# Kernel tuning notes

Hardware: AMD Instinct MI355X
Metric: run time of the kernel (lower is better)

Reference implementation:

```python
import jax, jax.numpy as jnp
import numpy as np

N_NODES = 100000
F_DIM = 128
D_LAT = 64
N_EDGES = 1000000
H_DIM = 128


def setup_inputs() -> dict:
    key = jax.random.key(0)
    ks = jax.random.split(key, 10)
    rng = np.random.default_rng(0)
    # positive edges (random graph) and non-edge negative pairs (dedup vs edge set,
    # mirroring the membership check in the torch elbo loop)
    edges = rng.integers(0, N_NODES, size=(2, N_EDGES))
    edge_hash = edges[0].astype(np.int64) * N_NODES + edges[1]
    cand = rng.integers(0, N_NODES, size=(2, 2 * N_EDGES))
    cand_hash = cand[0].astype(np.int64) * N_NODES + cand[1]
    keep = ~np.isin(cand_hash, edge_hash)
    neg = cand[:, keep][:, :N_EDGES]
    r = lambda k, s, sc=1.0: jax.random.normal(k, s, jnp.float32) * sc
    return {
        "x": r(ks[0], (N_NODES, F_DIM)),
        "eps": r(ks[1], (N_NODES, D_LAT)),
        "W_mu": r(ks[2], (F_DIM, D_LAT), 0.05),
        "b_mu": jnp.zeros((D_LAT,), jnp.float32),
        "W_lv": r(ks[3], (F_DIM, D_LAT), 0.05),
        "b_lv": jnp.zeros((D_LAT,), jnp.float32),
        "W1": r(ks[4], (D_LAT, H_DIM), 0.1),
        "b1": jnp.zeros((H_DIM,), jnp.float32),
        "W2": r(ks[5], (H_DIM, 1), 0.1),
        "b2": jnp.zeros((1,), jnp.float32),
        "edge_index": jnp.asarray(edges, jnp.int64) if jax.config.jax_enable_x64 else jnp.asarray(edges, jnp.int32),
        "neg_index": jnp.asarray(neg, jnp.int64) if jax.config.jax_enable_x64 else jnp.asarray(neg, jnp.int32),
    }


def reference(x, eps, W_mu, b_mu, W_lv, b_lv, W1, b1, W2, b2, edge_index, neg_index):
    # encoder: per-node diagonal Gaussian q(z|x)
    mu = x @ W_mu + b_mu            # [N, D]
    logvar = x @ W_lv + b_lv        # [N, D]
    z = mu + eps * jnp.exp(0.5 * logvar)  # q.rsample()

    def pair_logits(idx):
        zu = z[idx[0]]              # [E, D] gather
        zv = z[idx[1]]
        h = jax.nn.relu((zu * zv) @ W1 + b1)  # [E, H]
        return (h @ W2 + b2)[:, 0]  # [E]

    # Bernoulli(logits).log_prob(1) = log_sigmoid(l); log(1 - sigmoid(l)) = log_sigmoid(-l)
    true_lp = jax.nn.log_sigmoid(pair_logits(edge_index))
    false_lp = jax.nn.log_sigmoid(-pair_logits(neg_index))
    recon = jnp.mean(jnp.concatenate([true_lp, false_lp]))

    # KL(q || N(0, I)) per node, mean over nodes
    kl = jnp.mean(0.5 * jnp.sum(jnp.square(mu) + jnp.exp(logvar) - 1.0 - logvar, axis=-1))
    return -(recon - kl)
```

## Files before the change

kernel.cpp:

```cpp
#include <hip/hip_runtime.h>
#include <math.h>

#define F_DIM 128
#define D_LAT 64
#define H_DIM 128

typedef __attribute__((ext_vector_type(8))) short bf16x8;
typedef __attribute__((ext_vector_type(4))) float f32x4;
typedef __attribute__((ext_vector_type(2))) float f32x2;
typedef __attribute__((ext_vector_type(2))) unsigned long long u64x2;

__device__ __forceinline__ unsigned short f2bf(float f) {
    unsigned int u = __builtin_bit_cast(unsigned int, f);
    return (unsigned short)((u + 0x8000u) >> 16);
}

#define GLDS16(gaddr, laddr)                                                        \
    __builtin_amdgcn_global_load_lds(                                               \
        (const __attribute__((address_space(1))) void*)(gaddr),                     \
        (__attribute__((address_space(3))) void*)(laddr), 16, 0, 0)

__device__ __forceinline__ long prod_fp8(unsigned long long qu, unsigned long long qv) {
    const unsigned int ul = (unsigned int)qu, uh = (unsigned int)(qu >> 32);
    const unsigned int vl = (unsigned int)qv, vh = (unsigned int)(qv >> 32);
    const f32x2 u01 = __builtin_amdgcn_cvt_pk_f32_fp8(ul, false);
    const f32x2 u23 = __builtin_amdgcn_cvt_pk_f32_fp8(ul, true);
    const f32x2 u45 = __builtin_amdgcn_cvt_pk_f32_fp8(uh, false);
    const f32x2 u67 = __builtin_amdgcn_cvt_pk_f32_fp8(uh, true);
    const f32x2 v01 = __builtin_amdgcn_cvt_pk_f32_fp8(vl, false);
    const f32x2 v23 = __builtin_amdgcn_cvt_pk_f32_fp8(vl, true);
    const f32x2 v45 = __builtin_amdgcn_cvt_pk_f32_fp8(vh, false);
    const f32x2 v67 = __builtin_amdgcn_cvt_pk_f32_fp8(vh, true);
    const f32x2 p01 = u01 * v01, p23 = u23 * v23;
    const f32x2 p45 = u45 * v45, p67 = u67 * v67;
    unsigned int r0 = __builtin_amdgcn_cvt_pk_fp8_f32(p01[0], p01[1], 0u, false);
    r0 = __builtin_amdgcn_cvt_pk_fp8_f32(p23[0], p23[1], r0, true);
    unsigned int r1 = __builtin_amdgcn_cvt_pk_fp8_f32(p45[0], p45[1], 0u, false);
    r1 = __builtin_amdgcn_cvt_pk_fp8_f32(p67[0], p67[1], r1, true);
    return (long)(((unsigned long long)r1 << 32) | r0);
}

__global__ __launch_bounds__(256) void enc_mfma_kernel(
    const float* __restrict__ x, const float* __restrict__ eps,
    const float* __restrict__ Wmu, const float* __restrict__ bmu,
    const float* __restrict__ Wlv, const float* __restrict__ blv,
    unsigned char* __restrict__ zb, float* __restrict__ accum, int nNodes)
{
    const int lane = threadIdx.x & 63;
    const int li   = lane & 15;
    const int gi   = lane >> 4;

    bf16x8 wf[8][4];
#pragma unroll
    for (int t = 0; t < 4; ++t)
#pragma unroll
        for (int s = 0; s < 4; ++s)
#pragma unroll
            for (int j = 0; j < 8; ++j) {
                const int k = s * 32 + gi * 8 + j;
                wf[t][s][j]     = (short)f2bf(Wmu[k * D_LAT + 16 * t + li]);
                wf[t + 4][s][j] = (short)f2bf(Wlv[k * D_LAT + 16 * t + li]);
            }
    float bmu4[4], blv4[4];
#pragma unroll
    for (int t = 0; t < 4; ++t) {
        bmu4[t] = bmu[16 * t + li];
        blv4[t] = blv[16 * t + li];
    }

    const int wid = (blockIdx.x * blockDim.x + threadIdx.x) >> 6;
    const int nw  = (gridDim.x * blockDim.x) >> 6;
    const int NB  = nNodes >> 4;

    float klacc = 0.f;
    for (int nb = wid; nb < NB; nb += nw) {
        const int nbase = nb << 4;
        const float* __restrict__ xrow = x + (size_t)(nbase + li) * F_DIM;

        bf16x8 af[4];
#pragma unroll
        for (int s = 0; s < 4; ++s) {
            const f32x4 v0 = *(const f32x4*)(xrow + s * 32 + gi * 8);
            const f32x4 v1 = *(const f32x4*)(xrow + s * 32 + gi * 8 + 4);
#pragma unroll
            for (int j = 0; j < 4; ++j) {
                af[s][j]     = (short)f2bf(v0[j]);
                af[s][j + 4] = (short)f2bf(v1[j]);
            }
        }

        f32x4 acc[8];
#pragma unroll
        for (int t = 0; t < 4; ++t) {
            acc[t]     = (f32x4){bmu4[t], bmu4[t], bmu4[t], bmu4[t]};
            acc[t + 4] = (f32x4){blv4[t], blv4[t], blv4[t], blv4[t]};
        }
#pragma unroll
        for (int t = 0; t < 8; ++t)
#pragma unroll
            for (int s = 0; s < 4; ++s)
                acc[t] = __builtin_amdgcn_mfma_f32_16x16x32_bf16(af[s], wf[t][s], acc[t], 0, 0, 0);

#pragma unroll
        for (int r = 0; r < 4; ++r) {
            const int row = nbase + gi * 4 + r;
#pragma unroll
            for (int t = 0; t < 4; ++t) {
                const float mu  = acc[t][r];
                const float lv  = acc[t + 4][r];
                const float e05 = __expf(0.5f * lv);
                klacc += mu * mu + e05 * e05 - 1.0f - lv;
                const float zv = fmaf(eps[(size_t)row * D_LAT + 16 * t + li], e05, mu);
                zb[(size_t)row * D_LAT + 16 * t + li] =
                    (unsigned char)(__builtin_amdgcn_cvt_pk_fp8_f32(zv, 0.f, 0u, false) & 0xffu);
            }
        }
    }
    for (int off = 32; off; off >>= 1) klacc += __shfl_xor(klacc, off);
    if (lane == 0) atomicAdd(&accum[1], 0.5f * klacc);
}

__global__ __launch_bounds__(512) void edge_mfma_kernel(
    const unsigned char* __restrict__ zb,
    const int* __restrict__ eidx, const int* __restrict__ nidx,
    const float* __restrict__ W1, const float* __restrict__ b1,
    const float* __restrict__ W2, const float* __restrict__ b2,
    float* __restrict__ accum, int E)
{
    __shared__ unsigned char sh[8][2][4][1024];

    const int lane = threadIdx.x & 63;
    const int li   = lane & 15;
    const int gi   = lane >> 4;
    const int w    = threadIdx.x >> 6;

    long w1q[8][2];
#pragma unroll
    for (int t = 0; t < 8; ++t)
#pragma unroll
        for (int s = 0; s < 2; ++s) {
            float f[8];
#pragma unroll
            for (int j = 0; j < 8; ++j)
                f[j] = W1[(gi * 16 + s * 8 + j) * H_DIM + 16 * t + li];
            unsigned int r0 = __builtin_amdgcn_cvt_pk_fp8_f32(f[0], f[1], 0u, false);
            r0 = __builtin_amdgcn_cvt_pk_fp8_f32(f[2], f[3], r0, true);
            unsigned int r1 = __builtin_amdgcn_cvt_pk_fp8_f32(f[4], f[5], 0u, false);
            r1 = __builtin_amdgcn_cvt_pk_fp8_f32(f[6], f[7], r1, true);
            w1q[t][s] = (long)(((unsigned long long)r1 << 32) | r0);
        }
    float b1r[8], w2r[8];
#pragma unroll
    for (int t = 0; t < 8; ++t) {
        b1r[t] = b1[16 * t + li];
        w2r[t] = W2[16 * t + li];
    }
    const float b2v = b2[0];

    const int wid = (blockIdx.x * blockDim.x + threadIdx.x) >> 6;
    const int nw  = (gridDim.x * blockDim.x) >> 6;
    const int NBpos = E >> 4;
    const int NBH   = NBpos;

    float lp = 0.f;

    auto load_idx = [&](int hb, int& u0, int& v0, int& u1, int& v1) {
        const int h   = (hb < NBH) ? hb : (NBH - 1);
        const int pb0 = 2 * h, pb1 = 2 * h + 1;
        const int* __restrict__ i0 = (pb0 < NBpos) ? eidx : nidx;
        const int* __restrict__ i1 = (pb1 < NBpos) ? eidx : nidx;
        const int m0 = ((pb0 < NBpos) ? pb0 : pb0 - NBpos) << 4;
        const int m1 = ((pb1 < NBpos) ? pb1 : pb1 - NBpos) << 4;
        u0 = i0[m0 + li]; v0 = i0[E + m0 + li];
        u1 = i1[m1 + li]; v1 = i1[E + m1 + li];
    };
    auto stage = [&](int slot, int u0, int v0, int u1, int v1) {
        GLDS16(zb + (size_t)u0 * D_LAT + (gi << 4), &sh[w][slot][0][0]);
        GLDS16(zb + (size_t)v0 * D_LAT + (gi << 4), &sh[w][slot][1][0]);
        GLDS16(zb + (size_t)u1 * D_LAT + (gi << 4), &sh[w][slot][2][0]);
        GLDS16(zb + (size_t)v1 * D_LAT + (gi << 4), &sh[w][slot][3][0]);
    };
    auto do_block = [&](u64x2 qu, u64x2 qv, bool pos) {
        const long pa0 = prod_fp8(qu[0], qv[0]);
        const long pa1 = prod_fp8(qu[1], qv[1]);
        f32x4 acc[8];
#pragma unroll
        for (int t = 0; t < 8; ++t)
            acc[t] = (f32x4){b1r[t], b1r[t], b1r[t], b1r[t]};
#pragma unroll
        for (int t = 0; t < 8; ++t) {
            acc[t] = __builtin_amdgcn_mfma_f32_16x16x32_fp8_fp8(pa0, w1q[t][0], acc[t], 0, 0, 0);
            acc[t] = __builtin_amdgcn_mfma_f32_16x16x32_fp8_fp8(pa1, w1q[t][1], acc[t], 0, 0, 0);
        }
        float t0 = 0.f, t1 = 0.f, t2 = 0.f, t3 = 0.f;
#pragma unroll
        for (int t = 0; t < 8; ++t) {
            t0 += fmaxf(acc[t][0], 0.f) * w2r[t];
            t1 += fmaxf(acc[t][1], 0.f) * w2r[t];
            t2 += fmaxf(acc[t][2], 0.f) * w2r[t];
            t3 += fmaxf(acc[t][3], 0.f) * w2r[t];
        }
#pragma unroll
        for (int off = 1; off < 16; off <<= 1) {
            t0 += __shfl_xor(t0, off);
            t1 += __shfl_xor(t1, off);
            t2 += __shfl_xor(t2, off);
            t3 += __shfl_xor(t3, off);
        }
        const float sg = pos ? 1.f : -1.f;
        const float l0 = sg * (t0 + b2v), l1 = sg * (t1 + b2v);
        const float l2 = sg * (t2 + b2v), l3 = sg * (t3 + b2v);
        lp += fminf(l0, 0.f) - __logf(1.f + __expf(-fabsf(l0)));
        lp += fminf(l1, 0.f) - __logf(1.f + __expf(-fabsf(l1)));
        lp += fminf(l2, 0.f) - __logf(1.f + __expf(-fabsf(l2)));
        lp += fminf(l3, 0.f) - __logf(1.f + __expf(-fabsf(l3)));
    };

    int iu0, iv0, iu1, iv1;
    load_idx(wid, iu0, iv0, iu1, iv1);
    stage(0, iu0, iv0, iu1, iv1);
    load_idx(wid + nw, iu0, iv0, iu1, iv1);
    stage(1, iu0, iv0, iu1, iv1);
    load_idx(wid + 2 * nw, iu0, iv0, iu1, iv1);

    int slot = 0;
    for (int hb = wid; hb < NBH; hb += nw, slot ^= 1) {
        asm volatile("s_waitcnt vmcnt(8)" ::: "memory");
        const unsigned char* base = &sh[w][slot][0][0];
        const u64x2 qu0 = *(const u64x2*)(base + (lane << 4));
        const u64x2 qv0 = *(const u64x2*)(base + 1024 + (lane << 4));
        const u64x2 qu1 = *(const u64x2*)(base + 2048 + (lane << 4));
        const u64x2 qv1 = *(const u64x2*)(base + 3072 + (lane << 4));
        asm volatile("s_waitcnt lgkmcnt(0)" ::: "memory");

        int ju0, jv0, ju1, jv1;
        load_idx(hb + 3 * nw, ju0, jv0, ju1, jv1);
        stage(slot, iu0, iv0, iu1, iv1);
        iu0 = ju0; iv0 = jv0; iu1 = ju1; iv1 = jv1;

        do_block(qu0, qv0, 2 * hb < NBpos);
        do_block(qu1, qv1, 2 * hb + 1 < NBpos);
    }

    for (int off = 32; off; off >>= 1) lp += __shfl_xor(lp, off);
    if (lane == 0) atomicAdd(&accum[0], lp * 0.0625f);
}

__global__ void fin_kernel(const float* __restrict__ accum, float* __restrict__ out,
                           int nNodes, int E)
{
    const float recon = accum[0] / (float)(2 * E);
    const float kl    = accum[1] / (float)nNodes;
    out[0] = kl - recon;
}

extern "C" void kernel_launch(void* const* d_in, const int* in_sizes, int n_in,
                              void* d_out, int out_size, void* d_ws, size_t ws_size,
                              hipStream_t stream)
{
    const float* x    = (const float*)d_in[0];
    const float* eps  = (const float*)d_in[1];
    const float* Wmu  = (const float*)d_in[2];
    const float* bmu  = (const float*)d_in[3];
    const float* Wlv  = (const float*)d_in[4];
    const float* blv  = (const float*)d_in[5];
    const float* W1   = (const float*)d_in[6];
    const float* b1   = (const float*)d_in[7];
    const float* W2   = (const float*)d_in[8];
    const float* b2   = (const float*)d_in[9];
    const int*   eidx = (const int*)d_in[10];
    const int*   nidx = (const int*)d_in[11];

    const int nNodes = in_sizes[1] / D_LAT;
    const int E      = in_sizes[10] / 2;

    float* accum      = (float*)d_ws;
    unsigned char* zb = (unsigned char*)((char*)d_ws + 256);

    hipMemsetAsync(d_ws, 0, 256, stream);
    enc_mfma_kernel<<<512, 256, 0, stream>>>(x, eps, Wmu, bmu, Wlv, blv, zb, accum, nNodes);
    edge_mfma_kernel<<<512, 512, 0, stream>>>(zb, eidx, nidx, W1, b1, W2, b2, accum, E);
    fin_kernel<<<1, 1, 0, stream>>>(accum, (float*)d_out, nNodes, E);
}
```

Before: 179.4 us.

## Process one 16-edge block per iteration and raise edge-kernel occupancy

The edge kernel now handles a single 16-edge block per loop iteration instead of a pair, which halves the staged LDS footprint per wave and the number of gathers in flight. b1 and W2 move from per-thread registers into shared memory. Launch bounds become 256 threads with a minimum of 6 blocks per CU, and the grid grows to 1536 blocks. The aim is lower register and LDS pressure so more waves can hide gather latency, at the cost of less work per iteration and extra LDS reads for the bias and output weights.

```diff
diff --git a/kernel.cpp b/kernel.cpp
--- a/kernel.cpp
+++ b/kernel.cpp
@@ -120,19 +120,26 @@
     if (lane == 0) atomicAdd(&accum[1], 0.5f * klacc);
 }
 
-__global__ __launch_bounds__(512) void edge_mfma_kernel(
+__global__ __launch_bounds__(256, 6) void edge_mfma_kernel(
     const unsigned char* __restrict__ zb,
     const int* __restrict__ eidx, const int* __restrict__ nidx,
     const float* __restrict__ W1, const float* __restrict__ b1,
     const float* __restrict__ W2, const float* __restrict__ b2,
     float* __restrict__ accum, int E)
 {
-    __shared__ unsigned char sh[8][2][4][1024];
+    __shared__ unsigned char sh[4][2][2][1024];
+    __shared__ float bw[2][H_DIM];
 
     const int lane = threadIdx.x & 63;
     const int li   = lane & 15;
     const int gi   = lane >> 4;
     const int w    = threadIdx.x >> 6;
+
+    if (threadIdx.x < H_DIM) {
+        bw[0][threadIdx.x] = b1[threadIdx.x];
+        bw[1][threadIdx.x] = W2[threadIdx.x];
+    }
+    __syncthreads();
 
     long w1q[8][2];
 #pragma unroll
@@ -149,44 +156,34 @@
             r1 = __builtin_amdgcn_cvt_pk_fp8_f32(f[6], f[7], r1, true);
             w1q[t][s] = (long)(((unsigned long long)r1 << 32) | r0);
         }
-    float b1r[8], w2r[8];
-#pragma unroll
-    for (int t = 0; t < 8; ++t) {
-        b1r[t] = b1[16 * t + li];
-        w2r[t] = W2[16 * t + li];
-    }
     const float b2v = b2[0];
 
     const int wid = (blockIdx.x * blockDim.x + threadIdx.x) >> 6;
     const int nw  = (gridDim.x * blockDim.x) >> 6;
     const int NBpos = E >> 4;
-    const int NBH   = NBpos;
+    const int NBH   = NBpos << 1;
 
     float lp = 0.f;
 
-    auto load_idx = [&](int hb, int& u0, int& v0, int& u1, int& v1) {
-        const int h   = (hb < NBH) ? hb : (NBH - 1);
-        const int pb0 = 2 * h, pb1 = 2 * h + 1;
-        const int* __restrict__ i0 = (pb0 < NBpos) ? eidx : nidx;
-        const int* __restrict__ i1 = (pb1 < NBpos) ? eidx : nidx;
-        const int m0 = ((pb0 < NBpos) ? pb0 : pb0 - NBpos) << 4;
-        const int m1 = ((pb1 < NBpos) ? pb1 : pb1 - NBpos) << 4;
-        u0 = i0[m0 + li]; v0 = i0[E + m0 + li];
-        u1 = i1[m1 + li]; v1 = i1[E + m1 + li];
+    auto load_idx = [&](int hb, int& u, int& v) {
+        const int h = (hb < NBH) ? hb : (NBH - 1);
+        const int* __restrict__ ia = (h < NBpos) ? eidx : nidx;
+        const int m = ((h < NBpos) ? h : h - NBpos) << 4;
+        u = ia[m + li]; v = ia[E + m + li];
     };
-    auto stage = [&](int slot, int u0, int v0, int u1, int v1) {
-        GLDS16(zb + (size_t)u0 * D_LAT + (gi << 4), &sh[w][slot][0][0]);
-        GLDS16(zb + (size_t)v0 * D_LAT + (gi << 4), &sh[w][slot][1][0]);
-        GLDS16(zb + (size_t)u1 * D_LAT + (gi << 4), &sh[w][slot][2][0]);
-        GLDS16(zb + (size_t)v1 * D_LAT + (gi << 4), &sh[w][slot][3][0]);
+    auto stage = [&](int slot, int u, int v) {
+        GLDS16(zb + (size_t)u * D_LAT + (gi << 4), &sh[w][slot][0][0]);
+        GLDS16(zb + (size_t)v * D_LAT + (gi << 4), &sh[w][slot][1][0]);
     };
     auto do_block = [&](u64x2 qu, u64x2 qv, bool pos) {
         const long pa0 = prod_fp8(qu[0], qv[0]);
         const long pa1 = prod_fp8(qu[1], qv[1]);
         f32x4 acc[8];
 #pragma unroll
-        for (int t = 0; t < 8; ++t)
-            acc[t] = (f32x4){b1r[t], b1r[t], b1r[t], b1r[t]};
+        for (int t = 0; t < 8; ++t) {
+            const float bb = bw[0][16 * t + li];
+            acc[t] = (f32x4){bb, bb, bb, bb};
+        }
 #pragma unroll
         for (int t = 0; t < 8; ++t) {
             acc[t] = __builtin_amdgcn_mfma_f32_16x16x32_fp8_fp8(pa0, w1q[t][0], acc[t], 0, 0, 0);
@@ -195,10 +192,11 @@
         float t0 = 0.f, t1 = 0.f, t2 = 0.f, t3 = 0.f;
 #pragma unroll
         for (int t = 0; t < 8; ++t) {
-            t0 += fmaxf(acc[t][0], 0.f) * w2r[t];
-            t1 += fmaxf(acc[t][1], 0.f) * w2r[t];
-            t2 += fmaxf(acc[t][2], 0.f) * w2r[t];
-            t3 += fmaxf(acc[t][3], 0.f) * w2r[t];
+            const float w2v = bw[1][16 * t + li];
+            t0 += fmaxf(acc[t][0], 0.f) * w2v;
+            t1 += fmaxf(acc[t][1], 0.f) * w2v;
+            t2 += fmaxf(acc[t][2], 0.f) * w2v;
+            t3 += fmaxf(acc[t][3], 0.f) * w2v;
         }
 #pragma unroll
         for (int off = 1; off < 16; off <<= 1) {
@@ -216,30 +214,27 @@
         lp += fminf(l3, 0.f) - __logf(1.f + __expf(-fabsf(l3)));
     };
 
-    int iu0, iv0, iu1, iv1;
-    load_idx(wid, iu0, iv0, iu1, iv1);
-    stage(0, iu0, iv0, iu1, iv1);
-    load_idx(wid + nw, iu0, iv0, iu1, iv1);
-    stage(1, iu0, iv0, iu1, iv1);
-    load_idx(wid + 2 * nw, iu0, iv0, iu1, iv1);
+    int iu, iv;
+    load_idx(wid, iu, iv);
+    stage(0, iu, iv);
+    load_idx(wid + nw, iu, iv);
+    stage(1, iu, iv);
+    load_idx(wid + 2 * nw, iu, iv);
 
     int slot = 0;
     for (int hb = wid; hb < NBH; hb += nw, slot ^= 1) {
-        asm volatile("s_waitcnt vmcnt(8)" ::: "memory");
+        asm volatile("s_waitcnt vmcnt(4)" ::: "memory");
         const unsigned char* base = &sh[w][slot][0][0];
-        const u64x2 qu0 = *(const u64x2*)(base + (lane << 4));
-        const u64x2 qv0 = *(const u64x2*)(base + 1024 + (lane << 4));
-        const u64x2 qu1 = *(const u64x2*)(base + 2048 + (lane << 4));
-        const u64x2 qv1 = *(const u64x2*)(base + 3072 + (lane << 4));
+        const u64x2 qu = *(const u64x2*)(base + (lane << 4));
+        const u64x2 qv = *(const u64x2*)(base + 1024 + (lane << 4));
         asm volatile("s_waitcnt lgkmcnt(0)" ::: "memory");
 
-        int ju0, jv0, ju1, jv1;
-        load_idx(hb + 3 * nw, ju0, jv0, ju1, jv1);
-        stage(slot, iu0, iv0, iu1, iv1);
-        iu0 = ju0; iv0 = jv0; iu1 = ju1; iv1 = jv1;
-
-        do_block(qu0, qv0, 2 * hb < NBpos);
-        do_block(qu1, qv1, 2 * hb + 1 < NBpos);
+        int ju, jv;
+        load_idx(hb + 3 * nw, ju, jv);
+        stage(slot, iu, iv);
+        iu = ju; iv = jv;
+
+        do_block(qu, qv, hb < NBpos);
     }
 
     for (int off = 32; off; off >>= 1) lp += __shfl_xor(lp, off);
@@ -279,6 +274,6 @@
 
     hipMemsetAsync(d_ws, 0, 256, stream);
     enc_mfma_kernel<<<512, 256, 0, stream>>>(x, eps, Wmu, bmu, Wlv, blv, zb, accum, nNodes);
-    edge_mfma_kernel<<<512, 512, 0, stream>>>(zb, eidx, nidx, W1, b1, W2, b2, accum, E);
+    edge_mfma_kernel<<<1536, 256, 0, stream>>>(zb, eidx, nidx, W1, b1, W2, b2, accum, E);
     fin_kernel<<<1, 1, 0, stream>>>(accum, (float*)d_out, nNodes, E);
 }
```

New measurement: 201.8 us. 12.5% more time.

## Counting-sort edge pairs by source node before the edge MLP kernel

Applied to the files above, without the earlier changes.

Adds a histogram, a three-stage prefix scan and a scatter that bucket the positive and negative pairs by source node into a packed int2 array. The edge kernel then reads the sorted pairs, so consecutive warps gather the same or nearby z rows and should hit cache more often. The cost is several extra kernel launches, about 16MB of index traffic and heavy global atomics, all repeated on every call. An unsorted fallback is kept for when the workspace is too small.

```diff
diff --git a/kernel.cpp b/kernel.cpp
--- a/kernel.cpp
+++ b/kernel.cpp
@@ -4,6 +4,9 @@
 #define F_DIM 128
 #define D_LAT 64
 #define H_DIM 128
+#define NBINS 200000
+#define SCAN_B 256
+#define NSCAN_BLOCKS ((NBINS + SCAN_B - 1) / SCAN_B)
 
 typedef __attribute__((ext_vector_type(8))) short bf16x8;
 typedef __attribute__((ext_vector_type(4))) float f32x4;
@@ -120,9 +123,73 @@
     if (lane == 0) atomicAdd(&accum[1], 0.5f * klacc);
 }
 
+__global__ __launch_bounds__(256) void hist_kernel(
+    const int* __restrict__ eidx, const int* __restrict__ nidx,
+    int E, int nNodes, int* __restrict__ cnt)
+{
+    const int stride = gridDim.x * blockDim.x;
+    for (int i = blockIdx.x * blockDim.x + threadIdx.x; i < 2 * E; i += stride) {
+        if (i < E) atomicAdd(&cnt[eidx[i]], 1);
+        else       atomicAdd(&cnt[nNodes + nidx[i - E]], 1);
+    }
+}
+
+__global__ __launch_bounds__(SCAN_B) void scan1_kernel(
+    const int* __restrict__ cnt, int* __restrict__ off, int* __restrict__ bsum)
+{
+    __shared__ int s[SCAN_B];
+    const int t = threadIdx.x, i = blockIdx.x * SCAN_B + t;
+    const int v = (i < NBINS) ? cnt[i] : 0;
+    s[t] = v; __syncthreads();
+    for (int d = 1; d < SCAN_B; d <<= 1) {
+        const int add = (t >= d) ? s[t - d] : 0;
+        __syncthreads();
+        s[t] += add;
+        __syncthreads();
+    }
+    if (i < NBINS) off[i] = s[t] - v;
+    if (t == SCAN_B - 1) bsum[blockIdx.x] = s[t];
+}
+
+__global__ __launch_bounds__(1024) void scan2_kernel(int* __restrict__ bsum, int n)
+{
+    __shared__ int s[1024];
+    const int t = threadIdx.x;
+    const int v = (t < n) ? bsum[t] : 0;
+    s[t] = v; __syncthreads();
+    for (int d = 1; d < 1024; d <<= 1) {
+        const int add = (t >= d) ? s[t - d] : 0;
+        __syncthreads();
+        s[t] += add;
+        __syncthreads();
+    }
+    if (t < n) bsum[t] = s[t] - v;
+}
+
+__global__ __launch_bounds__(SCAN_B) void scan3_kernel(
+    int* __restrict__ off, const int* __restrict__ bsum)
+{
+    const int i = blockIdx.x * SCAN_B + threadIdx.x;
+    if (i < NBINS) off[i] += bsum[blockIdx.x];
+}
+
+__global__ __launch_bounds__(256) void scatter_kernel(
+    const int* __restrict__ eidx, const int* __restrict__ nidx,
+    int E, int nNodes, int* __restrict__ off, int2* __restrict__ suv)
+{
+    const int stride = gridDim.x * blockDim.x;
+    for (int i = blockIdx.x * blockDim.x + threadIdx.x; i < 2 * E; i += stride) {
+        int u, v, bin;
+        if (i < E) { u = eidx[i];     v = eidx[E + i];     bin = u; }
+        else       { u = nidx[i - E]; v = nidx[E + i - E]; bin = nNodes + u; }
+        const int p = atomicAdd(&off[bin], 1);
+        suv[p] = make_int2(u, v);
+    }
+}
+
 __global__ __launch_bounds__(512) void edge_mfma_kernel(
     const unsigned char* __restrict__ zb,
-    const int* __restrict__ eidx, const int* __restrict__ nidx,
+    const int2* __restrict__ suv,
     const float* __restrict__ W1, const float* __restrict__ b1,
     const float* __restrict__ W2, const float* __restrict__ b2,
     float* __restrict__ accum, int E)
@@ -162,6 +229,124 @@
     const int NBpos = E >> 4;
     const int NBH   = NBpos;
 
+    float lp = 0.f;
+
+    auto load_idx = [&](int hb, int& u0, int& v0, int& u1, int& v1) {
+        const int h  = (hb < NBH) ? hb : (NBH - 1);
+        const int m0 = (2 * h) << 4, m1 = (2 * h + 1) << 4;
+        const int2 a = suv[m0 + li];
+        const int2 b = suv[m1 + li];
+        u0 = a.x; v0 = a.y; u1 = b.x; v1 = b.y;
+    };
+    auto stage = [&](int slot, int u0, int v0, int u1, int v1) {
+        GLDS16(zb + (size_t)u0 * D_LAT + (gi << 4), &sh[w][slot][0][0]);
+        GLDS16(zb + (size_t)v0 * D_LAT + (gi << 4), &sh[w][slot][1][0]);
+        GLDS16(zb + (size_t)u1 * D_LAT + (gi << 4), &sh[w][slot][2][0]);
+        GLDS16(zb + (size_t)v1 * D_LAT + (gi << 4), &sh[w][slot][3][0]);
+    };
+    auto do_block = [&](u64x2 qu, u64x2 qv, bool pos) {
+        const long pa0 = prod_fp8(qu[0], qv[0]);
+        const long pa1 = prod_fp8(qu[1], qv[1]);
+        f32x4 acc[8];
+#pragma unroll
+        for (int t = 0; t < 8; ++t)
+            acc[t] = (f32x4){b1r[t], b1r[t], b1r[t], b1r[t]};
+#pragma unroll
+        for (int t = 0; t < 8; ++t) {
+            acc[t] = __builtin_amdgcn_mfma_f32_16x16x32_fp8_fp8(pa0, w1q[t][0], acc[t], 0, 0, 0);
+            acc[t] = __builtin_amdgcn_mfma_f32_16x16x32_fp8_fp8(pa1, w1q[t][1], acc[t], 0, 0, 0);
+        }
+        float t0 = 0.f, t1 = 0.f, t2 = 0.f, t3 = 0.f;
+#pragma unroll
+        for (int t = 0; t < 8; ++t) {
+            t0 += fmaxf(acc[t][0], 0.f) * w2r[t];
+            t1 += fmaxf(acc[t][1], 0.f) * w2r[t];
+            t2 += fmaxf(acc[t][2], 0.f) * w2r[t];
+            t3 += fmaxf(acc[t][3], 0.f) * w2r[t];
+        }
+#pragma unroll
+        for (int off = 1; off < 16; off <<= 1) {
+            t0 += __shfl_xor(t0, off);
+            t1 += __shfl_xor(t1, off);
+            t2 += __shfl_xor(t2, off);
+            t3 += __shfl_xor(t3, off);
+        }
+        const float sg = pos ? 1.f : -1.f;
+        const float l0 = sg * (t0 + b2v), l1 = sg * (t1 + b2v);
+        const float l2 = sg * (t2 + b2v), l3 = sg * (t3 + b2v);
+        lp += fminf(l0, 0.f) - __logf(1.f + __expf(-fabsf(l0)));
+        lp += fminf(l1, 0.f) - __logf(1.f + __expf(-fabsf(l1)));
+        lp += fminf(l2, 0.f) - __logf(1.f + __expf(-fabsf(l2)));
+        lp += fminf(l3, 0.f) - __logf(1.f + __expf(-fabsf(l3)));
+    };
+
+    int iu0, iv0, iu1, iv1;
+    load_idx(wid, iu0, iv0, iu1, iv1);
+    stage(0, iu0, iv0, iu1, iv1);
+    load_idx(wid + nw, iu0, iv0, iu1, iv1);
+    stage(1, iu0, iv0, iu1, iv1);
+    load_idx(wid + 2 * nw, iu0, iv0, iu1, iv1);
+
+    int slot = 0;
+    for (int hb = wid; hb < NBH; hb += nw, slot ^= 1) {
+        asm volatile("s_waitcnt vmcnt(6)" ::: "memory");
+        const unsigned char* base = &sh[w][slot][0][0];
+        const u64x2 qu0 = *(const u64x2*)(base + (lane << 4));
+        const u64x2 qv0 = *(const u64x2*)(base + 1024 + (lane << 4));
+        const u64x2 qu1 = *(const u64x2*)(base + 2048 + (lane << 4));
+        const u64x2 qv1 = *(const u64x2*)(base + 3072 + (lane << 4));
+        asm volatile("s_waitcnt lgkmcnt(0)" ::: "memory");
+
+        int ju0, jv0, ju1, jv1;
+        load_idx(hb + 3 * nw, ju0, jv0, ju1, jv1);
+        stage(slot, iu0, iv0, iu1, iv1);
+        iu0 = ju0; iv0 = jv0; iu1 = ju1; iv1 = jv1;
+
+        do_block(qu0, qv0, 2 * hb < NBpos);
+        do_block(qu1, qv1, 2 * hb + 1 < NBpos);
+    }
+
+    for (int off = 32; off; off >>= 1) lp += __shfl_xor(lp, off);
+    if (lane == 0) atomicAdd(&accum[0], lp * 0.0625f);
+}
+
+__global__ __launch_bounds__(512) void edge_legacy_kernel(
+    const unsigned char* __restrict__ zb,
+    const int* __restrict__ eidx, const int* __restrict__ nidx,
+    const float* __restrict__ W1, const float* __restrict__ b1,
+    const float* __restrict__ W2, const float* __restrict__ b2,
+    float* __restrict__ accum, int E)
+{
+    __shared__ unsigned char sh[8][2][4][1024];
+    const int lane = threadIdx.x & 63;
+    const int li   = lane & 15;
+    const int gi   = lane >> 4;
+    const int w    = threadIdx.x >> 6;
+
+    long w1q[8][2];
+#pragma unroll
+    for (int t = 0; t < 8; ++t)
+#pragma unroll
+        for (int s = 0; s < 2; ++s) {
+            float f[8];
+#pragma unroll
+            for (int j = 0; j < 8; ++j)
+                f[j] = W1[(gi * 16 + s * 8 + j) * H_DIM + 16 * t + li];
+            unsigned int r0 = __builtin_amdgcn_cvt_pk_fp8_f32(f[0], f[1], 0u, false);
+            r0 = __builtin_amdgcn_cvt_pk_fp8_f32(f[2], f[3], r0, true);
+            unsigned int r1 = __builtin_amdgcn_cvt_pk_fp8_f32(f[4], f[5], 0u, false);
+            r1 = __builtin_amdgcn_cvt_pk_fp8_f32(f[6], f[7], r1, true);
+            w1q[t][s] = (long)(((unsigned long long)r1 << 32) | r0);
+        }
+    float b1r[8], w2r[8];
+#pragma unroll
+    for (int t = 0; t < 8; ++t) { b1r[t] = b1[16 * t + li]; w2r[t] = W2[16 * t + li]; }
+    const float b2v = b2[0];
+
+    const int wid = (blockIdx.x * blockDim.x + threadIdx.x) >> 6;
+    const int nw  = (gridDim.x * blockDim.x) >> 6;
+    const int NBpos = E >> 4;
+    const int NBH   = NBpos;
     float lp = 0.f;
 
     auto load_idx = [&](int hb, int& u0, int& v0, int& u1, int& v1) {
@@ -185,8 +370,7 @@
         const long pa1 = prod_fp8(qu[1], qv[1]);
         f32x4 acc[8];
 #pragma unroll
-        for (int t = 0; t < 8; ++t)
-            acc[t] = (f32x4){b1r[t], b1r[t], b1r[t], b1r[t]};
+        for (int t = 0; t < 8; ++t) acc[t] = (f32x4){b1r[t], b1r[t], b1r[t], b1r[t]};
 #pragma unroll
         for (int t = 0; t < 8; ++t) {
             acc[t] = __builtin_amdgcn_mfma_f32_16x16x32_fp8_fp8(pa0, w1q[t][0], acc[t], 0, 0, 0);
@@ -202,10 +386,8 @@
         }
 #pragma unroll
         for (int off = 1; off < 16; off <<= 1) {
-            t0 += __shfl_xor(t0, off);
-            t1 += __shfl_xor(t1, off);
-            t2 += __shfl_xor(t2, off);
-            t3 += __shfl_xor(t3, off);
+            t0 += __shfl_xor(t0, off); t1 += __shfl_xor(t1, off);
+            t2 += __shfl_xor(t2, off); t3 += __shfl_xor(t3, off);
         }
         const float sg = pos ? 1.f : -1.f;
         const float l0 = sg * (t0 + b2v), l1 = sg * (t1 + b2v);
@@ -241,7 +423,6 @@
         do_block(qu0, qv0, 2 * hb < NBpos);
         do_block(qu1, qv1, 2 * hb + 1 < NBpos);
     }
-
     for (int off = 32; off; off >>= 1) lp += __shfl_xor(lp, off);
     if (lane == 0) atomicAdd(&accum[0], lp * 0.0625f);
 }
@@ -274,11 +455,28 @@
     const int nNodes = in_sizes[1] / D_LAT;
     const int E      = in_sizes[10] / 2;
 
-    float* accum      = (float*)d_ws;
-    unsigned char* zb = (unsigned char*)((char*)d_ws + 256);
-
-    hipMemsetAsync(d_ws, 0, 256, stream);
+    char* ws = (char*)d_ws;
+    float*         accum = (float*)ws;
+    unsigned char* zb    = (unsigned char*)(ws + 256);
+    int*           cnt   = (int*)(ws + 6400512);
+    int*           offb  = (int*)(ws + 7200512);
+    int*           bsum  = (int*)(ws + 8000512);
+    int2*          suv   = (int2*)(ws + 8004864);
+    const bool use_sort = ws_size >= (size_t)24100000;
+
+    hipMemsetAsync(accum, 0, 256, stream);
     enc_mfma_kernel<<<512, 256, 0, stream>>>(x, eps, Wmu, bmu, Wlv, blv, zb, accum, nNodes);
-    edge_mfma_kernel<<<512, 512, 0, stream>>>(zb, eidx, nidx, W1, b1, W2, b2, accum, E);
+
+    if (use_sort) {
+        hipMemsetAsync(cnt, 0, sizeof(int) * NBINS, stream);
+        hist_kernel<<<1024, 256, 0, stream>>>(eidx, nidx, E, nNodes, cnt);
+        scan1_kernel<<<NSCAN_BLOCKS, SCAN_B, 0, stream>>>(cnt, offb, bsum);
+        scan2_kernel<<<1, 1024, 0, stream>>>(bsum, NSCAN_BLOCKS);
+        scan3_kernel<<<NSCAN_BLOCKS, SCAN_B, 0, stream>>>(offb, bsum);
+        scatter_kernel<<<1024, 256, 0, stream>>>(eidx, nidx, E, nNodes, offb, suv);
+        edge_mfma_kernel<<<512, 512, 0, stream>>>(zb, suv, W1, b1, W2, b2, accum, E);
+    } else {
+        edge_legacy_kernel<<<512, 512, 0, stream>>>(zb, eidx, nidx, W1, b1, W2, b2, accum, E);
+    }
     fin_kernel<<<1, 1, 0, stream>>>(accum, (float*)d_out, nNodes, E);
 }
```

New measurement: 410.3 us. +128.7%, slower.
